# Performance work log

Hardware: AMD Instinct MI355X
Metric: run time of the kernel (lower is better)

The kernel has to match this reference:

```python
import jax, jax.numpy as jnp
import numpy as np

D_MODEL, D_KEY, D_VALUE, H = 1024, 64, 64, 16
B, S = 4, 2048

def setup_inputs() -> dict:
    key = jax.random.key(0)
    ks = jax.random.split(key, 11)
    sd = 1.0 / np.sqrt(D_MODEL)
    return {
        "queries": jax.random.normal(ks[0], (B, S, D_MODEL), jnp.float32),
        "keys": jax.random.normal(ks[1], (B, S, D_MODEL), jnp.float32),
        "values": jax.random.normal(ks[2], (B, S, D_MODEL), jnp.float32),
        "Wq": jax.random.normal(ks[3], (D_MODEL, H * D_KEY), jnp.float32) * sd,
        "bq": jax.random.normal(ks[4], (H * D_KEY,), jnp.float32) * 0.01,
        "Wk": jax.random.normal(ks[5], (D_MODEL, H * D_KEY), jnp.float32) * sd,
        "bk": jax.random.normal(ks[6], (H * D_KEY,), jnp.float32) * 0.01,
        "Wv": jax.random.normal(ks[7], (D_MODEL, H * D_VALUE), jnp.float32) * sd,
        "bv": jax.random.normal(ks[8], (H * D_VALUE,), jnp.float32) * 0.01,
        "Wo": jax.random.normal(ks[9], (H * D_VALUE, D_MODEL), jnp.float32) * sd,
        "bo": jax.random.normal(ks[10], (D_MODEL,), jnp.float32) * 0.01,
    }

def reference(queries, keys, values, Wq, bq, Wk, bk, Wv, bv, Wo, bo):
    bs, nq, _ = queries.shape
    nk = keys.shape[1]
    # projections -> [b, h, s, d]
    q = (queries @ Wq + bq).reshape(bs, nq, H, D_KEY).transpose(0, 2, 1, 3)
    k = (keys @ Wk + bk).reshape(bs, nk, H, D_KEY).transpose(0, 2, 1, 3)
    v = (values @ Wv + bv).reshape(bs, nk, H, D_VALUE).transpose(0, 2, 1, 3)
    att = jnp.einsum('bhqd,bhkd->bhqk', q, k) / np.sqrt(D_KEY).astype(np.float32)
    att = jax.nn.softmax(att, axis=-1)  # dropout is identity in eval mode
    out = jnp.einsum('bhqk,bhkd->bhqd', att, v)
    out = out.transpose(0, 2, 1, 3).reshape(bs, nq, H * D_VALUE)
    return out @ Wo + bo
```

## Files before the change

### kernel.cpp

```cpp
#include <hip/hip_runtime.h>
#include <hip/hip_bf16.h>
#include <stdint.h>

#define DM 1024
#define DKH 64
#define NH 16
#define NB 4
#define SEQ 2048

typedef __attribute__((ext_vector_type(8))) short bf16x8;
typedef __attribute__((ext_vector_type(4))) short bf16x4;
typedef __attribute__((ext_vector_type(8))) unsigned short ushort8;
typedef __attribute__((ext_vector_type(4))) float f32x4;

__device__ inline unsigned short f2bf(float f) {
  union { float f; unsigned u; } c; c.f = f;
  unsigned u = c.u;
  u += 0x7fff + ((u >> 16) & 1);
  return (unsigned short)(u >> 16);
}

#define GLOAD16(dst, ptr, OFF)                                              \
  asm volatile("global_load_dwordx4 %0, %1, off offset:" #OFF               \
               : "=v"(dst) : "v"(ptr))
#define GLOAD8(dst, ptr, OFF)                                               \
  asm volatile("global_load_dwordx2 %0, %1, off offset:" #OFF               \
               : "=v"(dst) : "v"(ptr))

#define WAITV(N)                                            \
  do {                                                      \
    asm volatile("s_waitcnt vmcnt(" #N ")" ::: "memory");   \
    __builtin_amdgcn_sched_barrier(0);                      \
  } while (0)

__device__ inline void mfma16x16x16(f32x4& acc, bf16x4 a, bf16x4 b) {
  asm("v_mfma_f32_16x16x16_bf16 %0, %1, %2, %0" : "+v"(acc) : "v"(a), "v"(b));
}

__global__ __launch_bounds__(256) void wcast_all(const float* __restrict__ W0,
                                                 const float* __restrict__ W1,
                                                 const float* __restrict__ W2,
                                                 const float* __restrict__ W3,
                                                 unsigned short* __restrict__ Wt0,
                                                 unsigned short* __restrict__ Wt1,
                                                 unsigned short* __restrict__ Wt2,
                                                 unsigned short* __restrict__ Wt3) {
  __shared__ float tile[32][33];
  int z = blockIdx.z;
  const float* W = z == 0 ? W0 : z == 1 ? W1 : z == 2 ? W2 : W3;
  unsigned short* Wt = z == 0 ? Wt0 : z == 1 ? Wt1 : z == 2 ? Wt2 : Wt3;
  int bk = blockIdx.x * 32, bn = blockIdx.y * 32;
  int tx = threadIdx.x & 31, ty = threadIdx.x >> 5;
#pragma unroll
  for (int i = 0; i < 4; ++i)
    tile[ty + 8 * i][tx] = W[(size_t)(bk + ty + 8 * i) * DM + bn + tx];
  __syncthreads();
#pragma unroll
  for (int i = 0; i < 4; ++i)
    Wt[(size_t)(bn + ty + 8 * i) * DM + bk + tx] = f2bf(tile[tx][ty + 8 * i]);
}

__global__ __launch_bounds__(256) void gemm_qkv(
    const float* __restrict__ Aq, const float* __restrict__ Ak,
    const float* __restrict__ Av, const unsigned short* __restrict__ Btq,
    const unsigned short* __restrict__ Btk, const unsigned short* __restrict__ Btv,
    const float* __restrict__ bq, const float* __restrict__ bk,
    const float* __restrict__ bv, unsigned short* __restrict__ Cq,
    unsigned short* __restrict__ Ck, unsigned short* __restrict__ Cv) {
  __shared__ __align__(16) unsigned short As[128][32];
  __shared__ __align__(16) unsigned short Bs[128][32];
  const int K = DM;
  int z = blockIdx.y;
  const float* A = z == 0 ? Aq : z == 1 ? Ak : Av;
  const unsigned short* Bt = z == 0 ? Btq : z == 1 ? Btk : Btv;
  const float* bias = z == 0 ? bq : z == 1 ? bk : bv;
  unsigned short* C = z == 0 ? Cq : z == 1 ? Ck : Cv;
  const float scale = z == 0 ? 0.125f * 1.4426950408889634f : 1.0f;

  int t = threadIdx.x;
  int wave = t >> 6, lane = t & 63;
  int wr = wave >> 1, wc = wave & 1;
  int l15 = lane & 15, g = lane >> 4;
  int tm = blockIdx.x >> 3, tn = blockIdx.x & 7;
  int rowBase = tm * 128, colBase = tn * 128;

  f32x4 acc[4][4];
#pragma unroll
  for (int mi = 0; mi < 4; ++mi)
#pragma unroll
    for (int ni = 0; ni < 4; ++ni) acc[mi][ni] = (f32x4){0.f, 0.f, 0.f, 0.f};

  int srow = t >> 2;
  int skb = (t & 3) * 8;

  for (int kt = 0; kt < K; kt += 32) {
    __syncthreads();
#pragma unroll
    for (int i = 0; i < 2; ++i) {
      int row = srow + i * 64;
      const float* Af = A + (size_t)(rowBase + row) * K + kt + skb;
      float4 x = *reinterpret_cast<const float4*>(Af);
      float4 y = *reinterpret_cast<const float4*>(Af + 4);
      ushort8 v;
      v[0] = f2bf(x.x); v[1] = f2bf(x.y); v[2] = f2bf(x.z); v[3] = f2bf(x.w);
      v[4] = f2bf(y.x); v[5] = f2bf(y.y); v[6] = f2bf(y.z); v[7] = f2bf(y.w);
      *reinterpret_cast<ushort8*>(&As[row][skb]) = v;
      ushort8 w = *reinterpret_cast<const ushort8*>(
          Bt + (size_t)(colBase + row) * K + kt + skb);
      *reinterpret_cast<ushort8*>(&Bs[row][skb]) = w;
    }
    __syncthreads();

    bf16x8 af[4], bfr[4];
#pragma unroll
    for (int mi = 0; mi < 4; ++mi)
      af[mi] = *reinterpret_cast<const bf16x8*>(&As[wr * 64 + mi * 16 + l15][g * 8]);
#pragma unroll
    for (int ni = 0; ni < 4; ++ni)
      bfr[ni] = *reinterpret_cast<const bf16x8*>(&Bs[wc * 64 + ni * 16 + l15][g * 8]);
#pragma unroll
    for (int mi = 0; mi < 4; ++mi)
#pragma unroll
      for (int ni = 0; ni < 4; ++ni)
        acc[mi][ni] = __builtin_amdgcn_mfma_f32_16x16x32_bf16(af[mi], bfr[ni],
                                                              acc[mi][ni], 0, 0, 0);
  }

#pragma unroll
  for (int ni = 0; ni < 4; ++ni) {
    int col = colBase + wc * 64 + ni * 16 + l15;
    float bvv = bias[col];
#pragma unroll
    for (int mi = 0; mi < 4; ++mi) {
#pragma unroll
      for (int r = 0; r < 4; ++r) {
        int row = rowBase + wr * 64 + mi * 16 + g * 4 + r;
        float val = (acc[mi][ni][r] + bvv) * scale;
        int b_ = row >> 11, s_ = row & 2047;
        int h_ = col >> 6, d_ = col & 63;
        size_t hb = (size_t)(b_ * NH + h_) * (SEQ * DKH);
        size_t idx;
        if (z == 0) {
          idx = hb + (size_t)s_ * DKH + d_;
        } else if (z == 1) {
          idx = hb + (size_t)(s_ >> 4) * 1024 + (d_ >> 5) * 512 +
                ((d_ >> 3) & 3) * 128 + (s_ & 15) * 8 + (d_ & 7);
        } else {
          idx = hb + (size_t)(s_ >> 5) * 2048 + ((s_ >> 4) & 1) * 1024 +
                (d_ >> 4) * 256 + ((s_ >> 2) & 3) * 64 + (d_ & 15) * 4 + (s_ & 3);
        }
        C[idx] = f2bf(val);
      }
    }
  }
}

__global__ __launch_bounds__(256) void gemm_out(const unsigned short* __restrict__ Ab,
                                                const unsigned short* __restrict__ Bt,
                                                const float* __restrict__ bias,
                                                float* __restrict__ C) {
  __shared__ __align__(16) unsigned short As[128][32];
  __shared__ __align__(16) unsigned short Bs[128][32];
  const int K = DM;
  int t = threadIdx.x;
  int wave = t >> 6, lane = t & 63;
  int wr = wave >> 1, wc = wave & 1;
  int l15 = lane & 15, g = lane >> 4;
  int tm = blockIdx.x >> 3, tn = blockIdx.x & 7;
  int rowBase = tm * 128, colBase = tn * 128;

  f32x4 acc[4][4];
#pragma unroll
  for (int mi = 0; mi < 4; ++mi)
#pragma unroll
    for (int ni = 0; ni < 4; ++ni) acc[mi][ni] = (f32x4){0.f, 0.f, 0.f, 0.f};

  int srow = t >> 2;
  int skb = (t & 3) * 8;

  for (int kt = 0; kt < K; kt += 32) {
    __syncthreads();
#pragma unroll
    for (int i = 0; i < 2; ++i) {
      int row = srow + i * 64;
      ushort8 v = *reinterpret_cast<const ushort8*>(
          Ab + (size_t)(rowBase + row) * K + kt + skb);
      *reinterpret_cast<ushort8*>(&As[row][skb]) = v;
      ushort8 w = *reinterpret_cast<const ushort8*>(
          Bt + (size_t)(colBase + row) * K + kt + skb);
      *reinterpret_cast<ushort8*>(&Bs[row][skb]) = w;
    }
    __syncthreads();

    bf16x8 af[4], bfr[4];
#pragma unroll
    for (int mi = 0; mi < 4; ++mi)
      af[mi] = *reinterpret_cast<const bf16x8*>(&As[wr * 64 + mi * 16 + l15][g * 8]);
#pragma unroll
    for (int ni = 0; ni < 4; ++ni)
      bfr[ni] = *reinterpret_cast<const bf16x8*>(&Bs[wc * 64 + ni * 16 + l15][g * 8]);
#pragma unroll
    for (int mi = 0; mi < 4; ++mi)
#pragma unroll
      for (int ni = 0; ni < 4; ++ni)
        acc[mi][ni] = __builtin_amdgcn_mfma_f32_16x16x32_bf16(af[mi], bfr[ni],
                                                              acc[mi][ni], 0, 0, 0);
  }

#pragma unroll
  for (int ni = 0; ni < 4; ++ni) {
    int col = colBase + wc * 64 + ni * 16 + l15;
    float bvv = bias[col];
#pragma unroll
    for (int mi = 0; mi < 4; ++mi)
#pragma unroll
      for (int r = 0; r < 4; ++r) {
        int row = rowBase + wr * 64 + mi * 16 + g * 4 + r;
        C[(size_t)row * DM + col] = acc[mi][ni][r] + bvv;
      }
  }
}

__global__ __launch_bounds__(256) void attn_fwd(const unsigned short* __restrict__ Qb,
                                                const unsigned short* __restrict__ Kp_,
                                                const unsigned short* __restrict__ Vp_,
                                                unsigned short* __restrict__ AO) {
  int t = threadIdx.x;
  int wave = t >> 6, lane = t & 63;
  int l15 = lane & 15, g = lane >> 4;
  int bid = blockIdx.x;
  int xcd = bid & 7, j = bid >> 3;
  int bh = (xcd << 3) | (j >> 4);
  int qtile = j & 15;
  const size_t baseH = (size_t)bh * SEQ * DKH;
  int q0 = qtile * 128 + wave * 32;

  bf16x8 aQ[2][2];
#pragma unroll
  for (int qf = 0; qf < 2; ++qf)
#pragma unroll
    for (int dh = 0; dh < 2; ++dh)
      aQ[qf][dh] = *reinterpret_cast<const bf16x8*>(
          Qb + baseH + (size_t)(q0 + qf * 16 + l15) * DKH + dh * 32 + g * 8);

  float m[2] = {-1e30f, -1e30f}, lsum[2] = {0.f, 0.f};
  f32x4 accO[2][4];
#pragma unroll
  for (int qf = 0; qf < 2; ++qf)
#pragma unroll
    for (int dt = 0; dt < 4; ++dt) accO[qf][dt] = (f32x4){0.f, 0.f, 0.f, 0.f};

  const unsigned short* kp = Kp_ + baseH + g * 128 + l15 * 8;
  const unsigned short* vp = Vp_ + baseH + g * 64 + l15 * 4;

  bf16x8 k0[2][2], k1[2][2], k2[2][2];
  bf16x4 v0[2][4], v1[2][4], v2[2][4];
  bf16x4 pf[2][2];

#define ISSUE_K(buf)                                  \
  do {                                                \
    GLOAD16(buf[0][0], kp, 0);                        \
    GLOAD16(buf[0][1], kp, 1024);                     \
    GLOAD16(buf[1][0], kp, 2048);                     \
    GLOAD16(buf[1][1], kp, 3072);                     \
    kp += 2048;                                       \
  } while (0)
#define ISSUE_V(buf)                                  \
  do {                                                \
    GLOAD8(buf[0][0], vp, 0);                         \
    GLOAD8(buf[0][1], vp, 512);                       \
    GLOAD8(buf[0][2], vp, 1024);                      \
    GLOAD8(buf[0][3], vp, 1536);                      \
    GLOAD8(buf[1][0], vp, 2048);                      \
    GLOAD8(buf[1][1], vp, 2560);                      \
    GLOAD8(buf[1][2], vp, 3072);                      \
    GLOAD8(buf[1][3], vp, 3584);                      \
    vp += 2048;                                       \
  } while (0)

  auto qksm = [&](const bf16x8 (&kf)[2][2]) {
    f32x4 sc[2][2];
#pragma unroll
    for (int qf = 0; qf < 2; ++qf)
#pragma unroll
      for (int tt = 0; tt < 2; ++tt) {
        f32x4 z = (f32x4){0.f, 0.f, 0.f, 0.f};
#pragma unroll
        for (int dh = 0; dh < 2; ++dh)
          z = __builtin_amdgcn_mfma_f32_16x16x32_bf16(kf[tt][dh], aQ[qf][dh], z, 0, 0, 0);
        sc[qf][tt] = z;
      }
#pragma unroll
    for (int qf = 0; qf < 2; ++qf) {
      float lm = fmaxf(
          fmaxf(fmaxf(sc[qf][0][0], sc[qf][0][1]), fmaxf(sc[qf][0][2], sc[qf][0][3])),
          fmaxf(fmaxf(sc[qf][1][0], sc[qf][1][1]), fmaxf(sc[qf][1][2], sc[qf][1][3])));
      if (__any(lm > m[qf] + 8.f)) {
        float vm = lm;
        vm = fmaxf(vm, __shfl_xor(vm, 16));
        vm = fmaxf(vm, __shfl_xor(vm, 32));
        float mnew = fmaxf(m[qf], vm);
        float alpha = __builtin_amdgcn_exp2f(m[qf] - mnew);
        m[qf] = mnew;
        lsum[qf] *= alpha;
#pragma unroll
        for (int dt = 0; dt < 4; ++dt)
#pragma unroll
          for (int r = 0; r < 4; ++r) accO[qf][dt][r] *= alpha;
      }
      float pv[8];
#pragma unroll
      for (int tt = 0; tt < 2; ++tt)
#pragma unroll
        for (int r = 0; r < 4; ++r)
          pv[tt * 4 + r] = __builtin_amdgcn_exp2f(sc[qf][tt][r] - m[qf]);
      lsum[qf] +=
          ((pv[0] + pv[1]) + (pv[2] + pv[3])) + ((pv[4] + pv[5]) + (pv[6] + pv[7]));
#pragma unroll
      for (int tt = 0; tt < 2; ++tt) {
        unsigned w0, w1;
        asm("v_cvt_pk_bf16_f32 %0, %1, %2"
            : "=v"(w0) : "v"(pv[tt * 4 + 0]), "v"(pv[tt * 4 + 1]));
        asm("v_cvt_pk_bf16_f32 %0, %1, %2"
            : "=v"(w1) : "v"(pv[tt * 4 + 2]), "v"(pv[tt * 4 + 3]));
        union { unsigned u[2]; bf16x4 v; } pk;
        pk.u[0] = w0; pk.u[1] = w1;
        pf[qf][tt] = pk.v;
      }
    }
  };

  auto pvstep = [&](const bf16x4 (&vf)[2][4]) {
#pragma unroll
    for (int qf = 0; qf < 2; ++qf)
#pragma unroll
      for (int tt = 0; tt < 2; ++tt)
#pragma unroll
        for (int dt = 0; dt < 4; ++dt)
          mfma16x16x16(accO[qf][dt], vf[tt][dt], pf[qf][tt]);
  };

  ISSUE_K(k0); ISSUE_V(v0);
  ISSUE_K(k1); ISSUE_V(v1);
  ISSUE_K(k2); ISSUE_V(v2);

  for (int it = 0; it < 21; ++it) {
    WAITV(32); qksm(k0); WAITV(24); pvstep(v0); ISSUE_K(k0); ISSUE_V(v0);
    WAITV(32); qksm(k1); WAITV(24); pvstep(v1); ISSUE_K(k1); ISSUE_V(v1);
    WAITV(32); qksm(k2); WAITV(24); pvstep(v2); ISSUE_K(k2); ISSUE_V(v2);
  }
  WAITV(32); qksm(k0); WAITV(24); pvstep(v0);
  WAITV(0);
#undef ISSUE_K
#undef ISSUE_V

  int b_ = bh >> 4, h_ = bh & 15;
#pragma unroll
  for (int qf = 0; qf < 2; ++qf) {
    float ls = lsum[qf];
    ls += __shfl_xor(ls, 16);
    ls += __shfl_xor(ls, 32);
    float inv = 1.f / ls;
    int sq = q0 + qf * 16 + l15;
#pragma unroll
    for (int dt = 0; dt < 4; ++dt)
#pragma unroll
      for (int r = 0; r < 4; ++r) {
        float val = accO[qf][dt][r] * inv;
        AO[(size_t)(b_ * SEQ + sq) * DM + h_ * DKH + dt * 16 + g * 4 + r] = f2bf(val);
      }
  }
}

extern "C" void kernel_launch(void* const* d_in, const int* in_sizes, int n_in,
                              void* d_out, int out_size, void* d_ws, size_t ws_size,
                              hipStream_t stream) {
  (void)in_sizes; (void)n_in; (void)out_size; (void)ws_size;
  const float* queries = (const float*)d_in[0];
  const float* keys = (const float*)d_in[1];
  const float* values = (const float*)d_in[2];
  const float* Wq = (const float*)d_in[3];
  const float* bq = (const float*)d_in[4];
  const float* Wk = (const float*)d_in[5];
  const float* bk = (const float*)d_in[6];
  const float* Wv = (const float*)d_in[7];
  const float* bv = (const float*)d_in[8];
  const float* Wo = (const float*)d_in[9];
  const float* bo = (const float*)d_in[10];
  float* out = (float*)d_out;

  char* ws = (char*)d_ws;
  unsigned short* wt_q = (unsigned short*)(ws + 0 * (1u << 21));
  unsigned short* wt_k = (unsigned short*)(ws + 1 * (1u << 21));
  unsigned short* wt_v = (unsigned short*)(ws + 2 * (1u << 21));
  unsigned short* wt_o = (unsigned short*)(ws + 3 * (1u << 21));
  unsigned short* Qb = (unsigned short*)(ws + (8u << 20));
  unsigned short* Kb = (unsigned short*)(ws + (24u << 20));
  unsigned short* Vt = (unsigned short*)(ws + (40u << 20));
  unsigned short* AO = (unsigned short*)(ws + (56u << 20));

  wcast_all<<<dim3(32, 32, 4), 256, 0, stream>>>(Wq, Wk, Wv, Wo,
                                                 wt_q, wt_k, wt_v, wt_o);
  gemm_qkv<<<dim3(512, 3), 256, 0, stream>>>(queries, keys, values,
                                             wt_q, wt_k, wt_v,
                                             bq, bk, bv, Qb, Kb, Vt);
  attn_fwd<<<1024, 256, 0, stream>>>(Qb, Kb, Vt, AO);
  gemm_out<<<512, 256, 0, stream>>>(AO, wt_o, bo, out);
}
```

Baseline: 269.3 us.

## Pre-cast activations to bf16 and stage GEMM tiles via direct global-to-LDS loads

```diff
diff --git a/kernel.cpp b/kernel.cpp
--- a/kernel.cpp
+++ b/kernel.cpp
@@ -33,8 +33,26 @@
     __builtin_amdgcn_sched_barrier(0);                      \
   } while (0)
 
+__device__ inline void glds16(const unsigned short* g, unsigned short* l) {
+  __builtin_amdgcn_global_load_lds(
+      (const __attribute__((address_space(1))) unsigned int*)g,
+      (__attribute__((address_space(3))) unsigned int*)l, 16, 0, 0);
+}
+
 __device__ inline void mfma16x16x16(f32x4& acc, bf16x4 a, bf16x4 b) {
   asm("v_mfma_f32_16x16x16_bf16 %0, %1, %2, %0" : "+v"(acc) : "v"(a), "v"(b));
+}
+
+__global__ __launch_bounds__(256) void acast(const float* __restrict__ A,
+                                             unsigned short* __restrict__ O) {
+  size_t i = ((size_t)blockIdx.x * 256 + threadIdx.x) * 8;
+  const float* p = A + i;
+  float4 x = *reinterpret_cast<const float4*>(p);
+  float4 y = *reinterpret_cast<const float4*>(p + 4);
+  ushort8 v;
+  v[0] = f2bf(x.x); v[1] = f2bf(x.y); v[2] = f2bf(x.z); v[3] = f2bf(x.w);
+  v[4] = f2bf(y.x); v[5] = f2bf(y.y); v[6] = f2bf(y.z); v[7] = f2bf(y.w);
+  *reinterpret_cast<ushort8*>(O + i) = v;
 }
 
 __global__ __launch_bounds__(256) void wcast_all(const float* __restrict__ W0,
@@ -60,105 +78,11 @@
     Wt[(size_t)(bn + ty + 8 * i) * DM + bk + tx] = f2bf(tile[tx][ty + 8 * i]);
 }
 
-__global__ __launch_bounds__(256) void gemm_qkv(
-    const float* __restrict__ Aq, const float* __restrict__ Ak,
-    const float* __restrict__ Av, const unsigned short* __restrict__ Btq,
-    const unsigned short* __restrict__ Btk, const unsigned short* __restrict__ Btv,
-    const float* __restrict__ bq, const float* __restrict__ bk,
-    const float* __restrict__ bv, unsigned short* __restrict__ Cq,
-    unsigned short* __restrict__ Ck, unsigned short* __restrict__ Cv) {
-  __shared__ __align__(16) unsigned short As[128][32];
-  __shared__ __align__(16) unsigned short Bs[128][32];
-  const int K = DM;
-  int z = blockIdx.y;
-  const float* A = z == 0 ? Aq : z == 1 ? Ak : Av;
-  const unsigned short* Bt = z == 0 ? Btq : z == 1 ? Btk : Btv;
-  const float* bias = z == 0 ? bq : z == 1 ? bk : bv;
-  unsigned short* C = z == 0 ? Cq : z == 1 ? Ck : Cv;
-  const float scale = z == 0 ? 0.125f * 1.4426950408889634f : 1.0f;
-
-  int t = threadIdx.x;
-  int wave = t >> 6, lane = t & 63;
-  int wr = wave >> 1, wc = wave & 1;
-  int l15 = lane & 15, g = lane >> 4;
-  int tm = blockIdx.x >> 3, tn = blockIdx.x & 7;
-  int rowBase = tm * 128, colBase = tn * 128;
-
-  f32x4 acc[4][4];
-#pragma unroll
-  for (int mi = 0; mi < 4; ++mi)
-#pragma unroll
-    for (int ni = 0; ni < 4; ++ni) acc[mi][ni] = (f32x4){0.f, 0.f, 0.f, 0.f};
-
-  int srow = t >> 2;
-  int skb = (t & 3) * 8;
-
-  for (int kt = 0; kt < K; kt += 32) {
-    __syncthreads();
-#pragma unroll
-    for (int i = 0; i < 2; ++i) {
-      int row = srow + i * 64;
-      const float* Af = A + (size_t)(rowBase + row) * K + kt + skb;
-      float4 x = *reinterpret_cast<const float4*>(Af);
-      float4 y = *reinterpret_cast<const float4*>(Af + 4);
-      ushort8 v;
-      v[0] = f2bf(x.x); v[1] = f2bf(x.y); v[2] = f2bf(x.z); v[3] = f2bf(x.w);
-      v[4] = f2bf(y.x); v[5] = f2bf(y.y); v[6] = f2bf(y.z); v[7] = f2bf(y.w);
-      *reinterpret_cast<ushort8*>(&As[row][skb]) = v;
-      ushort8 w = *reinterpret_cast<const ushort8*>(
-          Bt + (size_t)(colBase + row) * K + kt + skb);
-      *reinterpret_cast<ushort8*>(&Bs[row][skb]) = w;
-    }
-    __syncthreads();
-
-    bf16x8 af[4], bfr[4];
-#pragma unroll
-    for (int mi = 0; mi < 4; ++mi)
-      af[mi] = *reinterpret_cast<const bf16x8*>(&As[wr * 64 + mi * 16 + l15][g * 8]);
-#pragma unroll
-    for (int ni = 0; ni < 4; ++ni)
-      bfr[ni] = *reinterpret_cast<const bf16x8*>(&Bs[wc * 64 + ni * 16 + l15][g * 8]);
-#pragma unroll
-    for (int mi = 0; mi < 4; ++mi)
-#pragma unroll
-      for (int ni = 0; ni < 4; ++ni)
-        acc[mi][ni] = __builtin_amdgcn_mfma_f32_16x16x32_bf16(af[mi], bfr[ni],
-                                                              acc[mi][ni], 0, 0, 0);
-  }
-
-#pragma unroll
-  for (int ni = 0; ni < 4; ++ni) {
-    int col = colBase + wc * 64 + ni * 16 + l15;
-    float bvv = bias[col];
-#pragma unroll
-    for (int mi = 0; mi < 4; ++mi) {
-#pragma unroll
-      for (int r = 0; r < 4; ++r) {
-        int row = rowBase + wr * 64 + mi * 16 + g * 4 + r;
-        float val = (acc[mi][ni][r] + bvv) * scale;
-        int b_ = row >> 11, s_ = row & 2047;
-        int h_ = col >> 6, d_ = col & 63;
-        size_t hb = (size_t)(b_ * NH + h_) * (SEQ * DKH);
-        size_t idx;
-        if (z == 0) {
-          idx = hb + (size_t)s_ * DKH + d_;
-        } else if (z == 1) {
-          idx = hb + (size_t)(s_ >> 4) * 1024 + (d_ >> 5) * 512 +
-                ((d_ >> 3) & 3) * 128 + (s_ & 15) * 8 + (d_ & 7);
-        } else {
-          idx = hb + (size_t)(s_ >> 5) * 2048 + ((s_ >> 4) & 1) * 1024 +
-                (d_ >> 4) * 256 + ((s_ >> 2) & 3) * 64 + (d_ & 15) * 4 + (s_ & 3);
-        }
-        C[idx] = f2bf(val);
-      }
-    }
-  }
-}
-
-__global__ __launch_bounds__(256) void gemm_out(const unsigned short* __restrict__ Ab,
-                                                const unsigned short* __restrict__ Bt,
-                                                const float* __restrict__ bias,
-                                                float* __restrict__ C) {
+template <int EPI>
+__global__ __launch_bounds__(256) void gemm_bf16(const unsigned short* __restrict__ A,
+                                                 const unsigned short* __restrict__ Bt,
+                                                 const float* __restrict__ bias,
+                                                 void* __restrict__ Cv, float scale) {
   __shared__ __align__(16) unsigned short As[128][32];
   __shared__ __align__(16) unsigned short Bs[128][32];
   const int K = DM;
@@ -166,7 +90,10 @@
   int wave = t >> 6, lane = t & 63;
   int wr = wave >> 1, wc = wave & 1;
   int l15 = lane & 15, g = lane >> 4;
-  int tm = blockIdx.x >> 3, tn = blockIdx.x & 7;
+  int bid = blockIdx.x;
+  int xcd = bid & 7, ii = bid >> 3;
+  int tn = ii >> 3;
+  int tm = ((ii & 7) << 3) | xcd;
   int rowBase = tm * 128, colBase = tn * 128;
 
   f32x4 acc[4][4];
@@ -175,21 +102,25 @@
 #pragma unroll
     for (int ni = 0; ni < 4; ++ni) acc[mi][ni] = (f32x4){0.f, 0.f, 0.f, 0.f};
 
-  int srow = t >> 2;
-  int skb = (t & 3) * 8;
+  const unsigned short* sa0 =
+      A + (size_t)(rowBase + wave * 16 + (lane >> 2)) * K + (lane & 3) * 8;
+  const unsigned short* sa1 = sa0 + (size_t)64 * K;
+  const unsigned short* sb0 =
+      Bt + (size_t)(colBase + wave * 16 + (lane >> 2)) * K + (lane & 3) * 8;
+  const unsigned short* sb1 = sb0 + (size_t)64 * K;
+  unsigned short* la0 = &As[wave * 16][0];
+  unsigned short* la1 = &As[64 + wave * 16][0];
+  unsigned short* lb0 = &Bs[wave * 16][0];
+  unsigned short* lb1 = &Bs[64 + wave * 16][0];
 
   for (int kt = 0; kt < K; kt += 32) {
     __syncthreads();
-#pragma unroll
-    for (int i = 0; i < 2; ++i) {
-      int row = srow + i * 64;
-      ushort8 v = *reinterpret_cast<const ushort8*>(
-          Ab + (size_t)(rowBase + row) * K + kt + skb);
-      *reinterpret_cast<ushort8*>(&As[row][skb]) = v;
-      ushort8 w = *reinterpret_cast<const ushort8*>(
-          Bt + (size_t)(colBase + row) * K + kt + skb);
-      *reinterpret_cast<ushort8*>(&Bs[row][skb]) = w;
-    }
+    glds16(sa0, la0);
+    glds16(sa1, la1);
+    glds16(sb0, lb0);
+    glds16(sb1, lb1);
+    sa0 += 32; sa1 += 32; sb0 += 32; sb1 += 32;
+    WAITV(0);
     __syncthreads();
 
     bf16x8 af[4], bfr[4];
@@ -212,12 +143,31 @@
     int col = colBase + wc * 64 + ni * 16 + l15;
     float bvv = bias[col];
 #pragma unroll
-    for (int mi = 0; mi < 4; ++mi)
+    for (int mi = 0; mi < 4; ++mi) {
 #pragma unroll
       for (int r = 0; r < 4; ++r) {
         int row = rowBase + wr * 64 + mi * 16 + g * 4 + r;
-        C[(size_t)row * DM + col] = acc[mi][ni][r] + bvv;
-      }
+        float val = (acc[mi][ni][r] + bvv) * scale;
+        if (EPI == 3) {
+          ((float*)Cv)[(size_t)row * DM + col] = val;
+        } else {
+          int b_ = row >> 11, s_ = row & 2047;
+          int h_ = col >> 6, d_ = col & 63;
+          size_t hb = (size_t)(b_ * NH + h_) * (SEQ * DKH);
+          size_t idx;
+          if (EPI == 0) {
+            idx = hb + (size_t)s_ * DKH + d_;
+          } else if (EPI == 1) {
+            idx = hb + (size_t)(s_ >> 4) * 1024 + (d_ >> 5) * 512 +
+                  ((d_ >> 3) & 3) * 128 + (s_ & 15) * 8 + (d_ & 7);
+          } else {
+            idx = hb + (size_t)(s_ >> 5) * 2048 + ((s_ >> 4) & 1) * 1024 +
+                  (d_ >> 4) * 256 + ((s_ >> 2) & 3) * 64 + (d_ & 15) * 4 + (s_ & 3);
+          }
+          ((unsigned short*)Cv)[idx] = f2bf(val);
+        }
+      }
+    }
   }
 }
 
@@ -399,11 +349,16 @@
   unsigned short* Vt = (unsigned short*)(ws + (40u << 20));
   unsigned short* AO = (unsigned short*)(ws + (56u << 20));
 
+  const float SQ = 0.125f * 1.4426950408889634f;
+
   wcast_all<<<dim3(32, 32, 4), 256, 0, stream>>>(Wq, Wk, Wv, Wo,
                                                  wt_q, wt_k, wt_v, wt_o);
-  gemm_qkv<<<dim3(512, 3), 256, 0, stream>>>(queries, keys, values,
-                                             wt_q, wt_k, wt_v,
-                                             bq, bk, bv, Qb, Kb, Vt);
+  acast<<<4096, 256, 0, stream>>>(queries, AO);
+  gemm_bf16<0><<<512, 256, 0, stream>>>(AO, wt_q, bq, Qb, SQ);
+  acast<<<4096, 256, 0, stream>>>(keys, AO);
+  gemm_bf16<1><<<512, 256, 0, stream>>>(AO, wt_k, bk, Kb, 1.0f);
+  acast<<<4096, 256, 0, stream>>>(values, AO);
+  gemm_bf16<2><<<512, 256, 0, stream>>>(AO, wt_v, bv, Vt, 1.0f);
   attn_fwd<<<1024, 256, 0, stream>>>(Qb, Kb, Vt, AO);
-  gemm_out<<<512, 256, 0, stream>>>(AO, wt_o, bo, out);
-}
+  gemm_bf16<3><<<512, 256, 0, stream>>>(AO, wt_o, bo, out, 1.0f);
+}
```

Result: faster. 253.9 us (-5.7%).
